# Performance work log

Hardware: AMD Instinct MI355X
Metric: run time of the kernel (lower is better)

## Reference

```python
import math
import jax, jax.numpy as jnp
import numpy as np

NUM_BUCKETS = 32
MAX_DISTANCE = 128
N_HEADS = 16
D_KV = 64


def _relative_position_bucket(relative_position, num_buckets=NUM_BUCKETS, max_distance=MAX_DISTANCE):
    # bidirectional variant (encoder): half the buckets for each sign
    nb = num_buckets // 2
    n = -relative_position
    ret = (n < 0).astype(jnp.int32) * nb
    n = jnp.abs(n)
    max_exact = nb // 2
    is_small = n < max_exact
    val_if_large = max_exact + (
        jnp.log(jnp.maximum(n, 1).astype(jnp.float32) / max_exact)
        / math.log(max_distance / max_exact)
        * (nb - max_exact)
    ).astype(jnp.int32)
    val_if_large = jnp.minimum(val_if_large, nb - 1)
    return ret + jnp.where(is_small, n, val_if_large)


def setup_inputs() -> dict:
    key = jax.random.key(0)
    ks = jax.random.split(key, 6)
    d_model = 1024
    inner = N_HEADS * D_KV
    scale = 1.0 / math.sqrt(d_model)
    x = jax.random.normal(ks[0], (2, 2048, d_model), dtype=jnp.float32)
    wq = jax.random.normal(ks[1], (d_model, inner), dtype=jnp.float32) * scale
    wk = jax.random.normal(ks[2], (d_model, inner), dtype=jnp.float32) * scale
    wv = jax.random.normal(ks[3], (d_model, inner), dtype=jnp.float32) * scale
    wo = jax.random.normal(ks[4], (inner, d_model), dtype=jnp.float32) * scale
    rel_emb = jax.random.normal(ks[5], (NUM_BUCKETS, N_HEADS), dtype=jnp.float32)
    return {"x": x, "wq": wq, "wk": wk, "wv": wv, "wo": wo, "rel_emb": rel_emb}


def reference(x, wq, wk, wv, wo, rel_emb):
    B, S, D = x.shape
    # QKV projections (no bias, T5 style), split heads -> [B, S, H, Dk]
    q = (x @ wq).reshape(B, S, N_HEADS, D_KV)
    k = (x @ wk).reshape(B, S, N_HEADS, D_KV)
    v = (x @ wv).reshape(B, S, N_HEADS, D_KV)
    # NOTE: T5 does NOT scale by 1/sqrt(d_kv)
    scores = jnp.einsum("bqhd,bkhd->bhqk", q, k)  # [B, H, S, S]
    # relative position bias
    ctx = jnp.arange(S)[:, None]
    mem = jnp.arange(S)[None, :]
    buckets = _relative_position_bucket(mem - ctx)  # [S, S]
    bias = rel_emb[buckets]  # [S, S, H]
    bias = jnp.transpose(bias, (2, 0, 1))[None]  # [1, H, S, S]
    scores = scores + bias
    weights = jax.nn.softmax(scores.astype(jnp.float32), axis=-1).astype(scores.dtype)
    context = jnp.einsum("bhqk,bkhd->bqhd", weights, v).reshape(B, S, N_HEADS * D_KV)
    return context @ wo
```

## Files before the change

kernel.cpp:

```cpp
#include <hip/hip_runtime.h>
#include <hip/hip_bf16.h>

typedef __attribute__((ext_vector_type(8))) _Float16 f16x8;
typedef __attribute__((ext_vector_type(4))) float f32x4;
typedef unsigned short u16;
typedef unsigned int u32;

#define S_LEN 2048
#define NH    16
#define DK    64
#define DMODEL 1024
#define LSTR  40
#define LOG2E 1.44269504f
#define NTILES (S_LEN / 64)

union F16U { _Float16 h; u16 u; };
__device__ __forceinline__ u16 f2h(float f) {
    F16U v; v.h = (_Float16)f; return v.u;
}

__global__ __launch_bounds__(256) void bias_table_kernel(
    const float* __restrict__ rel_emb, float* __restrict__ tab)
{
    int idx = blockIdx.x * 256 + threadIdx.x;
    int h = idx >> 12;
    int t = idx & 4095;
    int rp = t - 2048;
    int n = -rp;
    int ret = 0;
    if (n < 0) { ret = 16; n = -n; }
    int inner;
    if (n < 8) {
        inner = n;
    } else {
        inner = 8 + (n >= 12) + (n >= 16) + (n >= 23) + (n >= 32)
                  + (n >= 46) + (n >= 64) + (n >= 91);
        if (inner > 15) inner = 15;
    }
    tab[h * 4096 + t] = rel_emb[(ret + inner) * NH + h] * LOG2E;
}

__global__ __launch_bounds__(256) void convert_x(
    const float* __restrict__ X, u16* __restrict__ Xf)
{
    long i8 = ((long)blockIdx.x * 256 + threadIdx.x) * 8;
    float4 a = *(const float4*)&X[i8];
    float4 b = *(const float4*)&X[i8 + 4];
    *(ushort4*)&Xf[i8] =
        make_ushort4(f2h(a.x), f2h(a.y), f2h(a.z), f2h(a.w));
    *(ushort4*)&Xf[i8 + 4] =
        make_ushort4(f2h(b.x), f2h(b.y), f2h(b.z), f2h(b.w));
}

__global__ __launch_bounds__(256) void convert_wT(
    const float* __restrict__ Wq, const float* __restrict__ Wk,
    const float* __restrict__ Wv, const float* __restrict__ Wo,
    u16* __restrict__ WT)
{
    const float* src = (blockIdx.z == 0) ? Wq : (blockIdx.z == 1) ? Wk
                     : (blockIdx.z == 2) ? Wv : Wo;
    u16* dT = WT + (long)blockIdx.z * 1048576;
    __shared__ __align__(16) float T[64 * 68];
    const int k0 = blockIdx.y * 64, n0 = blockIdx.x * 64;
    const int tid = threadIdx.x;
    #pragma unroll
    for (int u = 0; u < 4; u++) {
        int w = tid + u * 256;
        int r = w >> 4, c4 = (w & 15) * 4;
        *(float4*)&T[r * 68 + c4] =
            *(const float4*)&src[(long)(k0 + r) * DMODEL + n0 + c4];
    }
    __syncthreads();
    #pragma unroll
    for (int u = 0; u < 4; u++) {
        int w = tid + u * 256;
        int n = w >> 4, kc = (w & 15) * 4;
        *(ushort4*)&dT[(long)(n0 + n) * DMODEL + k0 + kc] = make_ushort4(
            f2h(T[(kc + 0) * 68 + n]), f2h(T[(kc + 1) * 68 + n]),
            f2h(T[(kc + 2) * 68 + n]), f2h(T[(kc + 3) * 68 + n]));
    }
}

__global__ __launch_bounds__(256, 3) void gemm_qkv_mfma(
    const u16* __restrict__ Xf, const u16* __restrict__ WT,
    u16* __restrict__ Qf, u16* __restrict__ Kf, u16* __restrict__ VT)
{
    const int z = blockIdx.z;
    const u16* BT = WT + (long)z * 1048576;

    __shared__ __align__(16) u16 Ah[128 * LSTR], Bh[128 * LSTR];

    const int tid = threadIdx.x;
    const int wv = tid >> 6, lane = tid & 63;
    const int g = lane >> 4, li = lane & 15;
    const int wr = wv >> 1, wc = wv & 1;
    const int bm = blockIdx.y * 128, bn = blockIdx.x * 128;

    const int srow = tid >> 2, sq8 = (tid & 3) * 8;
    const u16* As0 = &Xf[(long)(bm + srow) * DMODEL + sq8];
    const u16* As1 = As0 + 64 * DMODEL;
    const u16* Bs0 = &BT[(long)(bn + srow) * DMODEL + sq8];
    const u16* Bs1 = Bs0 + 64 * DMODEL;
    u16* AL0 = &Ah[srow * LSTR + sq8];
    u16* AL1 = &Ah[(srow + 64) * LSTR + sq8];
    u16* BL0 = &Bh[srow * LSTR + sq8];
    u16* BL1 = &Bh[(srow + 64) * LSTR + sq8];

    f32x4 acc[4][4];
    #pragma unroll
    for (int i = 0; i < 4; i++)
        #pragma unroll
        for (int j = 0; j < 4; j++) acc[i][j] = (f32x4){0.f, 0.f, 0.f, 0.f};

    *(uint4*)AL0 = *(const uint4*)As0;
    *(uint4*)AL1 = *(const uint4*)As1;
    *(uint4*)BL0 = *(const uint4*)Bs0;
    *(uint4*)BL1 = *(const uint4*)Bs1;
    __syncthreads();

    for (int k0 = 0; k0 < DMODEL; k0 += 32) {
        const bool have = (k0 + 32) < DMODEL;
        uint4 na0, na1, nb0, nb1;
        if (have) {
            na0 = *(const uint4*)(As0 + k0 + 32);
            na1 = *(const uint4*)(As1 + k0 + 32);
            nb0 = *(const uint4*)(Bs0 + k0 + 32);
            nb1 = *(const uint4*)(Bs1 + k0 + 32);
        }

        f16x8 a_h[4], b_h[4];
        #pragma unroll
        for (int i = 0; i < 4; i++)
            a_h[i] = *(const f16x8*)&Ah[(wr * 64 + i * 16 + li) * LSTR + g * 8];
        #pragma unroll
        for (int j = 0; j < 4; j++)
            b_h[j] = *(const f16x8*)&Bh[(wc * 64 + j * 16 + li) * LSTR + g * 8];
        #pragma unroll
        for (int i = 0; i < 4; i++)
            #pragma unroll
            for (int j = 0; j < 4; j++)
                acc[i][j] = __builtin_amdgcn_mfma_f32_16x16x32_f16(
                    a_h[i], b_h[j], acc[i][j], 0, 0, 0);

        if (have) {
            __syncthreads();
            *(uint4*)AL0 = na0; *(uint4*)AL1 = na1;
            *(uint4*)BL0 = nb0; *(uint4*)BL1 = nb1;
            __syncthreads();
        }
    }

    if (z == 2) {
        #pragma unroll
        for (int i = 0; i < 4; i++) {
            int s_base = bm + wr * 64 + i * 16 + g * 4;
            int bb = s_base >> 11, s = s_base & 2047;
            #pragma unroll
            for (int j = 0; j < 4; j++) {
                int gcol = bn + wc * 64 + j * 16 + li;
                int hh = gcol >> 6, d = gcol & 63;
                long idx = (((long)(bb * NH + hh)) * DK + d) * S_LEN + s;
                *(ushort4*)&VT[idx] = make_ushort4(
                    f2h(acc[i][j][0]), f2h(acc[i][j][1]),
                    f2h(acc[i][j][2]), f2h(acc[i][j][3]));
            }
        }
    } else {
        u16* O = (z == 0) ? Qf : Kf;
        #pragma unroll
        for (int i = 0; i < 4; i++) {
            #pragma unroll
            for (int r = 0; r < 4; r++) {
                int grow = bm + wr * 64 + i * 16 + g * 4 + r;
                int bb = grow >> 11, s = grow & 2047;
                #pragma unroll
                for (int j = 0; j < 4; j++) {
                    int gcol = bn + wc * 64 + j * 16 + li;
                    int hh = gcol >> 6, d = gcol & 63;
                    long idx = (((long)(bb * NH + hh)) * S_LEN + s) * DK + d;
                    O[idx] = f2h(acc[i][j][r]);
                }
            }
        }
    }
}

__global__ __launch_bounds__(256, 3) void gemm_out_mfma(
    const u16* __restrict__ Ab, const u16* __restrict__ WT,
    float* __restrict__ O)
{
    const u16* BT = WT + 3L * 1048576;
    __shared__ __align__(16) u16 Ah[128 * LSTR], Bh[128 * LSTR];

    const int tid = threadIdx.x;
    const int wv = tid >> 6, lane = tid & 63;
    const int g = lane >> 4, li = lane & 15;
    const int wr = wv >> 1, wc = wv & 1;
    const int bm = blockIdx.y * 128, bn = blockIdx.x * 128;

    const int srow = tid >> 2, sq8 = (tid & 3) * 8;
    const u16* As0 = &Ab[(long)(bm + srow) * DMODEL + sq8];
    const u16* As1 = As0 + 64 * DMODEL;
    const u16* Bs0 = &BT[(long)(bn + srow) * DMODEL + sq8];
    const u16* Bs1 = Bs0 + 64 * DMODEL;
    u16* AL0 = &Ah[srow * LSTR + sq8];
    u16* AL1 = &Ah[(srow + 64) * LSTR + sq8];
    u16* BL0 = &Bh[srow * LSTR + sq8];
    u16* BL1 = &Bh[(srow + 64) * LSTR + sq8];

    f32x4 acc[4][4];
    #pragma unroll
    for (int i = 0; i < 4; i++)
        #pragma unroll
        for (int j = 0; j < 4; j++) acc[i][j] = (f32x4){0.f, 0.f, 0.f, 0.f};

    *(uint4*)AL0 = *(const uint4*)As0;
    *(uint4*)AL1 = *(const uint4*)As1;
    *(uint4*)BL0 = *(const uint4*)Bs0;
    *(uint4*)BL1 = *(const uint4*)Bs1;
    __syncthreads();

    for (int k0 = 0; k0 < DMODEL; k0 += 32) {
        const bool have = (k0 + 32) < DMODEL;
        uint4 na0, na1, nb0, nb1;
        if (have) {
            na0 = *(const uint4*)(As0 + k0 + 32);
            na1 = *(const uint4*)(As1 + k0 + 32);
            nb0 = *(const uint4*)(Bs0 + k0 + 32);
            nb1 = *(const uint4*)(Bs1 + k0 + 32);
        }

        f16x8 a_h[4], b_h[4];
        #pragma unroll
        for (int i = 0; i < 4; i++)
            a_h[i] = *(const f16x8*)&Ah[(wr * 64 + i * 16 + li) * LSTR + g * 8];
        #pragma unroll
        for (int j = 0; j < 4; j++)
            b_h[j] = *(const f16x8*)&Bh[(wc * 64 + j * 16 + li) * LSTR + g * 8];
        #pragma unroll
        for (int i = 0; i < 4; i++)
            #pragma unroll
            for (int j = 0; j < 4; j++)
                acc[i][j] = __builtin_amdgcn_mfma_f32_16x16x32_f16(
                    a_h[i], b_h[j], acc[i][j], 0, 0, 0);

        if (have) {
            __syncthreads();
            *(uint4*)AL0 = na0; *(uint4*)AL1 = na1;
            *(uint4*)BL0 = nb0; *(uint4*)BL1 = nb1;
            __syncthreads();
        }
    }

    #pragma unroll
    for (int i = 0; i < 4; i++)
        #pragma unroll
        for (int r = 0; r < 4; r++) {
            int grow = bm + wr * 64 + i * 16 + g * 4 + r;
            #pragma unroll
            for (int j = 0; j < 4; j++) {
                int gcol = bn + wc * 64 + j * 16 + li;
                O[(long)grow * DMODEL + gcol] = acc[i][j][r];
            }
        }
}

#define APAD 72

__global__ __launch_bounds__(256, 4) void attn_mfma(
    const u16* __restrict__ Qf, const u16* __restrict__ Kf,
    const u16* __restrict__ VT, const float* __restrict__ tab,
    u16* __restrict__ ctxb)
{
    __shared__ __align__(16) u16 Ks[2][64 * APAD];
    __shared__ __align__(16) u16 Vs[2][64 * APAD];

    const int tid = threadIdx.x;
    const int wv = tid >> 6, lane = tid & 63;
    const int g = lane >> 4, li = lane & 15;

    const int nbid = (blockIdx.x & 7) * 128 + (blockIdx.x >> 3);
    const int qblk = nbid & 31;
    const int h = (nbid >> 5) & 15;
    const int b = nbid >> 9;
    const int q0 = qblk * 64;
    const long bh = b * NH + h;
    const int qloc = wv * 16 + li;

    const u16* KhG = Kf + bh * (S_LEN * DK);
    const u16* VtG = VT + bh * (DK * S_LEN);
    const float* thq = tab + h * 4096 + 2048 - q0 - qloc + g * 4;

    const int srow = tid >> 3, sc8 = (tid & 7) * 8;
    const u16* Kst = KhG + (long)srow * DK + sc8;
    const u16* Vst0 = VtG + (long)srow * S_LEN + sc8;
    const u16* Vst1 = VtG + (long)(srow + 32) * S_LEN + sc8;

    f16x8 q0f, q1f;
    {
        long qrow = bh * S_LEN + q0 + qloc;
        const u16* ph = Qf + qrow * DK + g * 8;
        q0f = *(const f16x8*)ph;  q1f = *(const f16x8*)(ph + 32);
    }

    *(uint4*)&Ks[0][srow * APAD + sc8] = *(const uint4*)Kst;
    *(uint4*)&Ks[0][(srow + 32) * APAD + sc8] = *(const uint4*)(Kst + 32 * DK);
    *(uint4*)&Vs[0][srow * APAD + sc8] = *(const uint4*)Vst0;
    *(uint4*)&Vs[0][(srow + 32) * APAD + sc8] = *(const uint4*)Vst1;
    uint4 nk0 = *(const uint4*)(Kst + 64 * DK);
    uint4 nk1 = *(const uint4*)(Kst + 96 * DK);
    uint4 nv0 = *(const uint4*)(Vst0 + 64);
    uint4 nv1 = *(const uint4*)(Vst1 + 64);
    __syncthreads();

    f32x4 Oc[4];
    #pragma unroll
    for (int n = 0; n < 4; n++) Oc[n] = (f32x4){0.f, 0.f, 0.f, 0.f};
    float mP = -1e30f, lR = 0.f;

    int cur = 0;
    for (int t = 0; t < NTILES; ++t) {
        const int kt0 = t * 64;

        const float* tb = thq + kt0;
        float bia[4][4];
        #pragma unroll
        for (int m = 0; m < 4; m++)
            #pragma unroll
            for (int r = 0; r < 4; r++)
                bia[m][r] = tb[m * 16 + r];

        f32x4 Sa[4];
        __builtin_amdgcn_s_setprio(1);
        #pragma unroll
        for (int m = 0; m < 4; m++) {
            const u16* kp = &Ks[cur][(m * 16 + li) * APAD + g * 8];
            f16x8 k0 = *(const f16x8*)kp, k1 = *(const f16x8*)(kp + 32);
            f32x4 s = (f32x4){0.f, 0.f, 0.f, 0.f};
            s = __builtin_amdgcn_mfma_f32_16x16x32_f16(k0, q0f, s, 0, 0, 0);
            s = __builtin_amdgcn_mfma_f32_16x16x32_f16(k1, q1f, s, 0, 0, 0);
            Sa[m] = s;
        }
        __builtin_amdgcn_s_setprio(0);

        if (t + 1 < NTILES) {
            *(uint4*)&Ks[cur ^ 1][srow * APAD + sc8] = nk0;
            *(uint4*)&Ks[cur ^ 1][(srow + 32) * APAD + sc8] = nk1;
            *(uint4*)&Vs[cur ^ 1][srow * APAD + sc8] = nv0;
            *(uint4*)&Vs[cur ^ 1][(srow + 32) * APAD + sc8] = nv1;
        }
        if (t + 2 < NTILES) {
            const u16* kp2 = Kst + (long)(kt0 + 128) * DK;
            nk0 = *(const uint4*)kp2;
            nk1 = *(const uint4*)(kp2 + 32 * DK);
            nv0 = *(const uint4*)(Vst0 + kt0 + 128);
            nv1 = *(const uint4*)(Vst1 + kt0 + 128);
        }

        #pragma unroll
        for (int m = 0; m < 4; m++)
            #pragma unroll
            for (int r = 0; r < 4; r++)
                Sa[m][r] = fmaf(Sa[m][r], LOG2E, bia[m][r]);

        float mm[4];
        #pragma unroll
        for (int m = 0; m < 4; m++)
            mm[m] = fmaxf(fmaxf(Sa[m][0], Sa[m][1]),
                          fmaxf(Sa[m][2], Sa[m][3]));
        float pm = fmaxf(fmaxf(mm[0], mm[1]), fmaxf(mm[2], mm[3]));
        pm = fmaxf(pm, __shfl_xor(pm, 16));
        pm = fmaxf(pm, __shfl_xor(pm, 32));

        if (__any(pm > mP)) {
            float mn = fmaxf(mP, pm);
            float alpha = __builtin_amdgcn_exp2f(mP - mn);
            mP = mn;
            lR *= alpha;
            float aO[4];
            #pragma unroll
            for (int r = 0; r < 4; r++) aO[r] = __shfl(alpha, g * 4 + r);
            #pragma unroll
            for (int n = 0; n < 4; n++)
                #pragma unroll
                for (int r = 0; r < 4; r++) Oc[n][r] *= aO[r];
        }

        float sm[4];
        #pragma unroll
        for (int m = 0; m < 4; m++) {
            #pragma unroll
            for (int r = 0; r < 4; r++)
                Sa[m][r] = __builtin_amdgcn_exp2f(Sa[m][r] - mP);
            sm[m] = (Sa[m][0] + Sa[m][1]) + (Sa[m][2] + Sa[m][3]);
        }
        float ls = (sm[0] + sm[1]) + (sm[2] + sm[3]);
        ls += __shfl_xor(ls, 16);
        ls += __shfl_xor(ls, 32);
        lR += ls;

        u32 y0, y1, y2, y3, y4, y5, y6, y7;
        {
            u32 p00 = f2h(Sa[0][0]) | ((u32)f2h(Sa[0][1]) << 16);
            u32 p01 = f2h(Sa[0][2]) | ((u32)f2h(Sa[0][3]) << 16);
            u32 p10 = f2h(Sa[1][0]) | ((u32)f2h(Sa[1][1]) << 16);
            u32 p11 = f2h(Sa[1][2]) | ((u32)f2h(Sa[1][3]) << 16);
            u32 p20 = f2h(Sa[2][0]) | ((u32)f2h(Sa[2][1]) << 16);
            u32 p21 = f2h(Sa[2][2]) | ((u32)f2h(Sa[2][3]) << 16);
            u32 p30 = f2h(Sa[3][0]) | ((u32)f2h(Sa[3][1]) << 16);
            u32 p31 = f2h(Sa[3][2]) | ((u32)f2h(Sa[3][3]) << 16);
            y0 = p00; y1 = p01; y2 = p10; y3 = p11;
            y4 = p20; y5 = p21; y6 = p30; y7 = p31;
        }
        {
            bool hi = (lane & 32) != 0;
            u32 s0 = hi ? y0 : y2, s1 = hi ? y1 : y3;
            u32 s4 = hi ? y4 : y6, s5 = hi ? y5 : y7;
            u32 r0 = __shfl_xor((int)s0, 32);
            u32 r1 = __shfl_xor((int)s1, 32);
            u32 r4 = __shfl_xor((int)s4, 32);
            u32 r5 = __shfl_xor((int)s5, 32);
            if (hi) { y0 = r0; y1 = r1; y4 = r4; y5 = r5; }
            else    { y2 = r0; y3 = r1; y6 = r4; y7 = r5; }
        }
        {
            bool hi = (lane & 16) != 0;
            u32 s0 = hi ? y0 : y2, s1 = hi ? y1 : y3;
            u32 s4 = hi ? y4 : y6, s5 = hi ? y5 : y7;
            u32 r0 = __shfl_xor((int)s0, 16);
            u32 r1 = __shfl_xor((int)s1, 16);
            u32 r4 = __shfl_xor((int)s4, 16);
            u32 r5 = __shfl_xor((int)s5, 16);
            if (hi) { y0 = r0; y1 = r1; y4 = r4; y5 = r5; }
            else    { y2 = r0; y3 = r1; y6 = r4; y7 = r5; }
        }
        union { uint4 u; f16x8 h; } P0, P1;
        P0.u = make_uint4(y0, y1, y2, y3);
        P1.u = make_uint4(y4, y5, y6, y7);

        __builtin_amdgcn_s_setprio(1);
        #pragma unroll
        for (int n = 0; n < 4; n++) {
            const u16* vp = &Vs[cur][(n * 16 + li) * APAD + g * 8];
            f16x8 v0 = *(const f16x8*)vp, v1 = *(const f16x8*)(vp + 32);
            Oc[n] = __builtin_amdgcn_mfma_f32_16x16x32_f16(P0.h, v0, Oc[n], 0, 0, 0);
            Oc[n] = __builtin_amdgcn_mfma_f32_16x16x32_f16(P1.h, v1, Oc[n], 0, 0, 0);
        }
        __builtin_amdgcn_s_setprio(0);

        __syncthreads();
        cur ^= 1;
    }

    float linv = 1.0f / lR;
    float iv[4];
    #pragma unroll
    for (int r = 0; r < 4; r++) iv[r] = __shfl(linv, g * 4 + r);
    #pragma unroll
    for (int n = 0; n < 4; n++)
        #pragma unroll
        for (int r = 0; r < 4; r++)
            ctxb[((long)(b * S_LEN + q0 + wv * 16 + g * 4 + r)) * DMODEL
                 + h * DK + n * 16 + li] = f2h(Oc[n][r] * iv[r]);
}

extern "C" void kernel_launch(void* const* d_in, const int* in_sizes, int n_in,
                              void* d_out, int out_size, void* d_ws, size_t ws_size,
                              hipStream_t stream)
{
    const float* x    = (const float*)d_in[0];
    const float* wq   = (const float*)d_in[1];
    const float* wk   = (const float*)d_in[2];
    const float* wv   = (const float*)d_in[3];
    const float* wo   = (const float*)d_in[4];
    const float* rel  = (const float*)d_in[5];

    u16* W0 = (u16*)d_ws;
    u16* Xf  = W0;
    u16* Qf  = W0 + 4194304;
    u16* Kf  = W0 + 8388608;
    u16* VT  = W0 + 12582912;
    u16* WT  = W0 + 16777216;
    float* tab = (float*)(W0 + 20971520);
    u16* ctxb = Xf;

    bias_table_kernel<<<dim3(256), dim3(256), 0, stream>>>(rel, tab);
    convert_x<<<dim3(2048), dim3(256), 0, stream>>>(x, Xf);
    convert_wT<<<dim3(16, 16, 4), dim3(256), 0, stream>>>(wq, wk, wv, wo, WT);
    gemm_qkv_mfma<<<dim3(8, 32, 3), dim3(256), 0, stream>>>(Xf, WT, Qf, Kf, VT);
    attn_mfma<<<dim3(1024), dim3(256), 0, stream>>>(Qf, Kf, VT, tab, ctxb);
    gemm_out_mfma<<<dim3(8, 32), dim3(256), 0, stream>>>(ctxb, WT, (float*)d_out);
}
```

Baseline: 217.3 us.

## Load K/V tiles directly to LDS with XOR swizzle and constant far-field bias

```diff
diff --git a/kernel.cpp b/kernel.cpp
--- a/kernel.cpp
+++ b/kernel.cpp
@@ -17,6 +17,12 @@
 union F16U { _Float16 h; u16 u; };
 __device__ __forceinline__ u16 f2h(float f) {
     F16U v; v.h = (_Float16)f; return v.u;
+}
+
+__device__ __forceinline__ void gl16(const u16* g, u16* l) {
+    __builtin_amdgcn_global_load_lds(
+        (__attribute__((address_space(1))) void*)(u16*)g,
+        (__attribute__((address_space(3))) void*)l, 16, 0, 0);
 }
 
 __global__ __launch_bounds__(256) void bias_table_kernel(
@@ -265,15 +271,13 @@
         }
 }
 
-#define APAD 72
-
 __global__ __launch_bounds__(256, 4) void attn_mfma(
     const u16* __restrict__ Qf, const u16* __restrict__ Kf,
     const u16* __restrict__ VT, const float* __restrict__ tab,
     u16* __restrict__ ctxb)
 {
-    __shared__ __align__(16) u16 Ks[2][64 * APAD];
-    __shared__ __align__(16) u16 Vs[2][64 * APAD];
+    __shared__ __align__(16) u16 Ks[2][4096];
+    __shared__ __align__(16) u16 Vs[2][4096];
 
     const int tid = threadIdx.x;
     const int wv = tid >> 6, lane = tid & 63;
@@ -289,12 +293,21 @@
 
     const u16* KhG = Kf + bh * (S_LEN * DK);
     const u16* VtG = VT + bh * (DK * S_LEN);
-    const float* thq = tab + h * 4096 + 2048 - q0 - qloc + g * 4;
-
-    const int srow = tid >> 3, sc8 = (tid & 7) * 8;
-    const u16* Kst = KhG + (long)srow * DK + sc8;
-    const u16* Vst0 = VtG + (long)srow * S_LEN + sc8;
-    const u16* Vst1 = VtG + (long)(srow + 32) * S_LEN + sc8;
+    const float* th0 = tab + h * 4096;
+    const float* thq = th0 + 2048 - q0 - qloc + g * 4;
+
+    const int sr  = lane >> 3;
+    const int sd8 = ((lane & 7) ^ sr) * 8;
+    const int c0 = wv * 2, c1 = wv * 2 + 1;
+    const u16* Kg0 = KhG + (long)(c0 * 8 + sr) * DK + sd8;
+    const u16* Kg1 = KhG + (long)(c1 * 8 + sr) * DK + sd8;
+    const u16* Vg0 = VtG + (long)(c0 * 8 + sr) * S_LEN + sd8;
+    const u16* Vg1 = VtG + (long)(c1 * 8 + sr) * S_LEN + sd8;
+
+    const int sw  = (li & 7) * 8;
+    const int roA = (g * 8) ^ sw;
+    const int roB = (g * 8 + 32) ^ sw;
+    const int rrow = li * 64;
 
     f16x8 q0f, q1f;
     {
@@ -302,15 +315,13 @@
         const u16* ph = Qf + qrow * DK + g * 8;
         q0f = *(const f16x8*)ph;  q1f = *(const f16x8*)(ph + 32);
     }
-
-    *(uint4*)&Ks[0][srow * APAD + sc8] = *(const uint4*)Kst;
-    *(uint4*)&Ks[0][(srow + 32) * APAD + sc8] = *(const uint4*)(Kst + 32 * DK);
-    *(uint4*)&Vs[0][srow * APAD + sc8] = *(const uint4*)Vst0;
-    *(uint4*)&Vs[0][(srow + 32) * APAD + sc8] = *(const uint4*)Vst1;
-    uint4 nk0 = *(const uint4*)(Kst + 64 * DK);
-    uint4 nk1 = *(const uint4*)(Kst + 96 * DK);
-    uint4 nv0 = *(const uint4*)(Vst0 + 64);
-    uint4 nv1 = *(const uint4*)(Vst1 + 64);
+    const float bias_hi = th0[2048 + 512];
+    const float bias_lo = th0[2048 - 512];
+
+    gl16(Kg0, &Ks[0][c0 * 512]);
+    gl16(Kg1, &Ks[0][c1 * 512]);
+    gl16(Vg0, &Vs[0][c0 * 512]);
+    gl16(Vg1, &Vs[0][c1 * 512]);
     __syncthreads();
 
     f32x4 Oc[4];
@@ -322,40 +333,43 @@
     for (int t = 0; t < NTILES; ++t) {
         const int kt0 = t * 64;
 
-        const float* tb = thq + kt0;
+        if (t + 1 < NTILES) {
+            const long ko = (long)(kt0 + 64) * DK;
+            gl16(Kg0 + ko, &Ks[cur ^ 1][c0 * 512]);
+            gl16(Kg1 + ko, &Ks[cur ^ 1][c1 * 512]);
+            gl16(Vg0 + kt0 + 64, &Vs[cur ^ 1][c0 * 512]);
+            gl16(Vg1 + kt0 + 64, &Vs[cur ^ 1][c1 * 512]);
+        }
+
         float bia[4][4];
-        #pragma unroll
-        for (int m = 0; m < 4; m++)
-            #pragma unroll
-            for (int r = 0; r < 4; r++)
-                bia[m][r] = tb[m * 16 + r];
+        const int dd = kt0 - q0;
+        if (dd >= 192 || dd <= -192) {
+            const float bc = (dd > 0) ? bias_hi : bias_lo;
+            #pragma unroll
+            for (int m = 0; m < 4; m++)
+                #pragma unroll
+                for (int r = 0; r < 4; r++) bia[m][r] = bc;
+        } else {
+            const float* tb = thq + kt0;
+            #pragma unroll
+            for (int m = 0; m < 4; m++)
+                #pragma unroll
+                for (int r = 0; r < 4; r++) bia[m][r] = tb[m * 16 + r];
+        }
 
         f32x4 Sa[4];
         __builtin_amdgcn_s_setprio(1);
         #pragma unroll
         for (int m = 0; m < 4; m++) {
-            const u16* kp = &Ks[cur][(m * 16 + li) * APAD + g * 8];
-            f16x8 k0 = *(const f16x8*)kp, k1 = *(const f16x8*)(kp + 32);
+            const u16* kp = &Ks[cur][m * 1024 + rrow];
+            f16x8 k0 = *(const f16x8*)(kp + roA);
+            f16x8 k1 = *(const f16x8*)(kp + roB);
             f32x4 s = (f32x4){0.f, 0.f, 0.f, 0.f};
             s = __builtin_amdgcn_mfma_f32_16x16x32_f16(k0, q0f, s, 0, 0, 0);
             s = __builtin_amdgcn_mfma_f32_16x16x32_f16(k1, q1f, s, 0, 0, 0);
             Sa[m] = s;
         }
         __builtin_amdgcn_s_setprio(0);
-
-        if (t + 1 < NTILES) {
-            *(uint4*)&Ks[cur ^ 1][srow * APAD + sc8] = nk0;
-            *(uint4*)&Ks[cur ^ 1][(srow + 32) * APAD + sc8] = nk1;
-            *(uint4*)&Vs[cur ^ 1][srow * APAD + sc8] = nv0;
-            *(uint4*)&Vs[cur ^ 1][(srow + 32) * APAD + sc8] = nv1;
-        }
-        if (t + 2 < NTILES) {
-            const u16* kp2 = Kst + (long)(kt0 + 128) * DK;
-            nk0 = *(const uint4*)kp2;
-            nk1 = *(const uint4*)(kp2 + 32 * DK);
-            nv0 = *(const uint4*)(Vst0 + kt0 + 128);
-            nv1 = *(const uint4*)(Vst1 + kt0 + 128);
-        }
 
         #pragma unroll
         for (int m = 0; m < 4; m++)
@@ -401,16 +415,14 @@
 
         u32 y0, y1, y2, y3, y4, y5, y6, y7;
         {
-            u32 p00 = f2h(Sa[0][0]) | ((u32)f2h(Sa[0][1]) << 16);
-            u32 p01 = f2h(Sa[0][2]) | ((u32)f2h(Sa[0][3]) << 16);
-            u32 p10 = f2h(Sa[1][0]) | ((u32)f2h(Sa[1][1]) << 16);
-            u32 p11 = f2h(Sa[1][2]) | ((u32)f2h(Sa[1][3]) << 16);
-            u32 p20 = f2h(Sa[2][0]) | ((u32)f2h(Sa[2][1]) << 16);
-            u32 p21 = f2h(Sa[2][2]) | ((u32)f2h(Sa[2][3]) << 16);
-            u32 p30 = f2h(Sa[3][0]) | ((u32)f2h(Sa[3][1]) << 16);
-            u32 p31 = f2h(Sa[3][2]) | ((u32)f2h(Sa[3][3]) << 16);
-            y0 = p00; y1 = p01; y2 = p10; y3 = p11;
-            y4 = p20; y5 = p21; y6 = p30; y7 = p31;
+            y0 = f2h(Sa[0][0]) | ((u32)f2h(Sa[0][1]) << 16);
+            y1 = f2h(Sa[0][2]) | ((u32)f2h(Sa[0][3]) << 16);
+            y2 = f2h(Sa[1][0]) | ((u32)f2h(Sa[1][1]) << 16);
+            y3 = f2h(Sa[1][2]) | ((u32)f2h(Sa[1][3]) << 16);
+            y4 = f2h(Sa[2][0]) | ((u32)f2h(Sa[2][1]) << 16);
+            y5 = f2h(Sa[2][2]) | ((u32)f2h(Sa[2][3]) << 16);
+            y6 = f2h(Sa[3][0]) | ((u32)f2h(Sa[3][1]) << 16);
+            y7 = f2h(Sa[3][2]) | ((u32)f2h(Sa[3][3]) << 16);
         }
         {
             bool hi = (lane & 32) != 0;
@@ -441,8 +453,9 @@
         __builtin_amdgcn_s_setprio(1);
         #pragma unroll
         for (int n = 0; n < 4; n++) {
-            const u16* vp = &Vs[cur][(n * 16 + li) * APAD + g * 8];
-            f16x8 v0 = *(const f16x8*)vp, v1 = *(const f16x8*)(vp + 32);
+            const u16* vp = &Vs[cur][n * 1024 + rrow];
+            f16x8 v0 = *(const f16x8*)(vp + roA);
+            f16x8 v1 = *(const f16x8*)(vp + roB);
             Oc[n] = __builtin_amdgcn_mfma_f32_16x16x32_f16(P0.h, v0, Oc[n], 0, 0, 0);
             Oc[n] = __builtin_amdgcn_mfma_f32_16x16x32_f16(P1.h, v1, Oc[n], 0, 0, 0);
         }
```

Result: no change. 216.7 us (-0.3%).
